# Kernel tuning notes

Measured on AMD Instinct MI355X. Metric: run time of the kernel, lower is better.

## Reference

```python
import math
import jax, jax.numpy as jnp
import numpy as np

B, L, INPUT_DIM, OUTPUT_DIM = 16, 4096, 7, 1
D_MODEL, N_HEADS, E_LAYERS, D_FF = 512, 8, 3, 2048
FACTOR, PRED_WIN = 5, 48


def layer_norm(x, g, b, eps=1e-5):
    m = x.mean(-1, keepdims=True)
    v = ((x - m) ** 2).mean(-1, keepdims=True)
    return (x - m) / jnp.sqrt(v + eps) * g + b


def prob_attention(q, k, v, key):
    # q,k,v: [B,H,L,d].  Canonical Informer ProbAttention, mask_flag=False.
    Bq, H, Lq, d = q.shape
    Lk = k.shape[2]
    sample_k = min(FACTOR * int(math.ceil(math.log(Lk))), Lk)
    n_top = min(FACTOR * int(math.ceil(math.log(Lq))), Lq)
    idx = jax.random.randint(key, (Lq, sample_k), 0, Lk)  # sampled key ids per query
    # sparsity measure M = max_s(QK_s) - mean(QK_s); indices carry no gradient
    qs = jax.lax.stop_gradient(q)
    ksg = jax.lax.stop_gradient(k)
    def body(carry, idx_s):
        m, s = carry
        ks = ksg[:, :, idx_s, :]                       # [B,H,Lq,d] gather
        qk = jnp.einsum('bhld,bhld->bhl', qs, ks)
        return (jnp.maximum(m, qk), s + qk), None
    init = (jnp.full((Bq, H, Lq), -jnp.inf, q.dtype), jnp.zeros((Bq, H, Lq), q.dtype))
    (m, s), _ = jax.lax.scan(body, init, idx.T)
    M = m - s / Lk
    top_idx = jax.lax.top_k(M, n_top)[1]               # [B,H,u] active queries
    q_red = jnp.take_along_axis(q, top_idx[..., None], axis=2)  # [B,H,u,d]
    scores = jnp.einsum('bhud,bhkd->bhuk', q_red, k) / jnp.sqrt(jnp.asarray(d, q.dtype))
    attn = jax.nn.softmax(scores, axis=-1)
    upd = jnp.einsum('bhuk,bhkd->bhud', attn, v)
    ctx = jnp.broadcast_to(v.mean(axis=2, keepdims=True), (Bq, H, Lq, d))
    bi = jnp.arange(Bq)[:, None, None]
    hi = jnp.arange(H)[None, :, None]
    return ctx.at[bi, hi, top_idx].set(upd)


def encoder_layer(x, Wq, bq, Wk, bk, Wv, bv, Wo, bo, W1, b1, W2, b2, g1, be1, g2, be2, key):
    Bx, Lx, D = x.shape
    H, d = N_HEADS, D // N_HEADS
    q = (x @ Wq + bq).reshape(Bx, Lx, H, d).transpose(0, 2, 1, 3)
    k = (x @ Wk + bk).reshape(Bx, Lx, H, d).transpose(0, 2, 1, 3)
    v = (x @ Wv + bv).reshape(Bx, Lx, H, d).transpose(0, 2, 1, 3)
    ctx = prob_attention(q, k, v, key)
    new_x = ctx.transpose(0, 2, 1, 3).reshape(Bx, Lx, D) @ Wo + bo
    x = layer_norm(x + new_x, g1, be1)
    y = jax.nn.gelu(x @ W1.T + b1, approximate=False)   # conv1d k=1 == linear
    y = y @ W2.T + b2
    return layer_norm(x + y, g2, be2)


def conv_layer(x, W, b, bn_g, bn_b):
    # Conv1d k=3 circular pad -> eval BatchNorm (mean 0, var 1) -> ELU -> MaxPool k=3 s=2 p=1
    xt = jnp.transpose(x, (0, 2, 1))                   # [B,C,L]
    xp = jnp.concatenate([xt[..., -1:], xt, xt[..., :1]], axis=-1)
    y = jax.lax.conv_general_dilated(xp, W, (1,), 'VALID', dimension_numbers=('NCH', 'OIH', 'NCH'))
    y = y + b[None, :, None]
    y = y / jnp.sqrt(1.0 + 1e-5) * bn_g[None, :, None] + bn_b[None, :, None]
    y = jax.nn.elu(y)
    yp = jnp.pad(y, ((0, 0), (0, 0), (1, 1)), constant_values=-jnp.inf)
    y = jax.lax.reduce_window(yp, -jnp.inf, jax.lax.max, (1, 1, 3), (1, 1, 2), 'VALID')
    return jnp.transpose(y, (0, 2, 1))                 # [B,L//2,C]


def setup_inputs() -> dict:
    key = jax.random.key(0)
    ks = jax.random.split(key, 12)
    s = 0.02
    f32 = jnp.float32
    return {
        'x': jax.random.normal(ks[0], (B, L, INPUT_DIM), f32),
        'emb_W': jax.random.normal(ks[1], (INPUT_DIM, D_MODEL), f32) * s,
        'emb_b': jnp.zeros((D_MODEL,), f32),
        'Wq': jax.random.normal(ks[2], (E_LAYERS, D_MODEL, D_MODEL), f32) * s,
        'bq': jnp.zeros((E_LAYERS, D_MODEL), f32),
        'Wk': jax.random.normal(ks[3], (E_LAYERS, D_MODEL, D_MODEL), f32) * s,
        'bk': jnp.zeros((E_LAYERS, D_MODEL), f32),
        'Wv': jax.random.normal(ks[4], (E_LAYERS, D_MODEL, D_MODEL), f32) * s,
        'bv': jnp.zeros((E_LAYERS, D_MODEL), f32),
        'Wo': jax.random.normal(ks[5], (E_LAYERS, D_MODEL, D_MODEL), f32) * s,
        'bo': jnp.zeros((E_LAYERS, D_MODEL), f32),
        'ff_W1': jax.random.normal(ks[6], (E_LAYERS, D_FF, D_MODEL), f32) * s,
        'ff_b1': jnp.zeros((E_LAYERS, D_FF), f32),
        'ff_W2': jax.random.normal(ks[7], (E_LAYERS, D_MODEL, D_FF), f32) * s,
        'ff_b2': jnp.zeros((E_LAYERS, D_MODEL), f32),
        'ln1_g': jnp.ones((E_LAYERS, D_MODEL), f32),
        'ln1_b': jnp.zeros((E_LAYERS, D_MODEL), f32),
        'ln2_g': jnp.ones((E_LAYERS, D_MODEL), f32),
        'ln2_b': jnp.zeros((E_LAYERS, D_MODEL), f32),
        'conv_W': jax.random.normal(ks[8], (E_LAYERS - 1, D_MODEL, D_MODEL, 3), f32) * s,
        'conv_b': jnp.zeros((E_LAYERS - 1, D_MODEL), f32),
        'bn_g': jnp.ones((E_LAYERS - 1, D_MODEL), f32),
        'bn_b': jnp.zeros((E_LAYERS - 1, D_MODEL), f32),
        'fln_g': jnp.ones((D_MODEL,), f32),
        'fln_b': jnp.zeros((D_MODEL,), f32),
        'proj_W': jax.random.normal(ks[9], (D_MODEL, OUTPUT_DIM), f32) * s,
        'proj_b': jnp.zeros((OUTPUT_DIM,), f32),
    }


def reference(x, emb_W, emb_b, Wq, bq, Wk, bk, Wv, bv, Wo, bo, ff_W1, ff_b1, ff_W2, ff_b2,
              ln1_g, ln1_b, ln2_g, ln2_b, conv_W, conv_b, bn_g, bn_b, fln_g, fln_b, proj_W, proj_b):
    h = x @ emb_W + emb_b
    base = jax.random.key(42)
    for i in range(E_LAYERS):
        h = encoder_layer(h, Wq[i], bq[i], Wk[i], bk[i], Wv[i], bv[i], Wo[i], bo[i],
                          ff_W1[i], ff_b1[i], ff_W2[i], ff_b2[i],
                          ln1_g[i], ln1_b[i], ln2_g[i], ln2_b[i],
                          jax.random.fold_in(base, i))
        if i < E_LAYERS - 1:
            h = conv_layer(h, conv_W[i], conv_b[i], bn_g[i], bn_b[i])
    h = layer_norm(h, fln_g, fln_b)
    out = h @ proj_W + proj_b
    return out[:, :PRED_WIN - 1, :]
```

## Files before the change

### kernel.cpp

```cpp
#include <hip/hip_runtime.h>
#include <cstdint>
#include <math.h>

#define NB 16
#define DM 512
#define NH 8
#define DFF_ 2048
#define SMAX 45

typedef unsigned short ushort_t;
typedef __bf16 bf16x8 __attribute__((ext_vector_type(8)));
typedef float f32x4 __attribute__((ext_vector_type(4)));

__device__ __forceinline__ ushort_t f2b(float f) {
  uint32_t u = __float_as_uint(f);
  uint32_t r = (u + 0x7FFFu + ((u >> 16) & 1u)) >> 16;
  return (ushort_t)r;
}
__device__ __forceinline__ float bu2f(ushort_t x) {
  return __uint_as_float((uint32_t)x << 16);
}
__device__ __forceinline__ float b2f_lo(uint32_t u) { return __uint_as_float(u << 16); }
__device__ __forceinline__ float b2f_hi(uint32_t u) { return __uint_as_float(u & 0xFFFF0000u); }
__device__ __forceinline__ uint32_t pack2(float lo, float hi) {
  return (uint32_t)f2b(lo) | ((uint32_t)f2b(hi) << 16);
}

__host__ __device__ inline void tf2x32(uint32_t k0, uint32_t k1,
                                       uint32_t x0, uint32_t x1,
                                       uint32_t* o0, uint32_t* o1) {
  uint32_t ks0 = k0, ks1 = k1, ks2 = k0 ^ k1 ^ 0x1BD11BDAu;
  x0 += ks0; x1 += ks1;
#define TF_RND(r) { x0 += x1; x1 = (x1 << (r)) | (x1 >> (32 - (r))); x1 ^= x0; }
  TF_RND(13) TF_RND(15) TF_RND(26) TF_RND(6)
  x0 += ks1; x1 += ks2 + 1u;
  TF_RND(17) TF_RND(29) TF_RND(16) TF_RND(24)
  x0 += ks2; x1 += ks0 + 2u;
  TF_RND(13) TF_RND(15) TF_RND(26) TF_RND(6)
  x0 += ks0; x1 += ks1 + 3u;
  TF_RND(17) TF_RND(29) TF_RND(16) TF_RND(24)
  x0 += ks1; x1 += ks2 + 4u;
  TF_RND(13) TF_RND(15) TF_RND(26) TF_RND(6)
  x0 += ks2; x1 += ks0 + 5u;
#undef TF_RND
  *o0 = x0; *o1 = x1;
}

__global__ void gen_idx_kernel(int* __restrict__ idx, uint32_t k0, uint32_t k1,
                               int n, int mask) {
  int j = blockIdx.x * 256 + threadIdx.x;
  if (j >= n) return;
  int half = n >> 1;
  uint32_t o0, o1;
  if (j < half) {
    tf2x32(k0, k1, (uint32_t)j, (uint32_t)(j + half), &o0, &o1);
    idx[j] = (int)(o0 & (uint32_t)mask);
  } else {
    tf2x32(k0, k1, (uint32_t)(j - half), (uint32_t)j, &o0, &o1);
    idx[j] = (int)(o1 & (uint32_t)mask);
  }
}

__device__ inline float blk_reduce_sum(float v) {
  __shared__ float s[4];
  for (int o = 32; o > 0; o >>= 1) v += __shfl_down(v, o);
  int lane = threadIdx.x & 63, w = threadIdx.x >> 6;
  if (lane == 0) s[w] = v;
  __syncthreads();
  float r = s[0] + s[1] + s[2] + s[3];
  __syncthreads();
  return r;
}

__global__ void embed_kernel(const float* __restrict__ x, const float* __restrict__ W,
                             const float* __restrict__ bias, ushort_t* __restrict__ h) {
  size_t gid = (size_t)blockIdx.x * 256 + threadIdx.x;
  int o4 = (int)(gid & 127) * 4;
  size_t bl = gid >> 7;
  const float* xr = x + bl * 7;
  float xv[7];
#pragma unroll
  for (int i = 0; i < 7; ++i) xv[i] = xr[i];
  float4 acc = *(const float4*)(bias + o4);
#pragma unroll
  for (int i = 0; i < 7; ++i) {
    float4 w4 = *(const float4*)(W + i * 512 + o4);
    acc.x += xv[i] * w4.x;
    acc.y += xv[i] * w4.y;
    acc.z += xv[i] * w4.z;
    acc.w += xv[i] * w4.w;
  }
  ushort4 o;
  o.x = f2b(acc.x); o.y = f2b(acc.y); o.z = f2b(acc.z); o.w = f2b(acc.w);
  *(ushort4*)(h + bl * 512 + o4) = o;
}

__global__ void cast_bf16(const float* __restrict__ src, ushort_t* __restrict__ dst,
                          size_t n) {
  size_t i = ((size_t)blockIdx.x * 256 + threadIdx.x) * 4;
  if (i >= n) return;
  float4 v = *(const float4*)(src + i);
  ushort4 o;
  o.x = f2b(v.x); o.y = f2b(v.y); o.z = f2b(v.z); o.w = f2b(v.w);
  *(ushort4*)(dst + i) = o;
}

__global__ void castT512(const float* __restrict__ W, ushort_t* __restrict__ Bt) {
  int gid = blockIdx.x * 256 + threadIdx.x;
  int n = gid >> 9, k = gid & 511;
  Bt[gid] = f2b(W[(size_t)k * 512 + n]);
}

__global__ void cast_convW(const float* __restrict__ W, ushort_t* __restrict__ Bt) {
  int gid = blockIdx.x * 256 + threadIdx.x;
  int n = gid / 1536, k = gid - n * 1536;
  int dt = k >> 9, ii = k & 511;
  Bt[gid] = f2b(W[((size_t)n * 512 + ii) * 3 + dt]);
}

__global__ void concat3(const float* __restrict__ a, const float* __restrict__ b,
                        const float* __restrict__ c, float* __restrict__ o) {
  int t = blockIdx.x * 256 + threadIdx.x;
  if (t >= 1536) return;
  o[t] = t < 512 ? a[t] : (t < 1024 ? b[t - 512] : c[t - 1024]);
}

__device__ __forceinline__ float gelu_exact(float c) {
  return 0.5f * c * (1.0f + erff(c * 0.70710678118654752f));
}

template <int MODE, int EPI>
__global__ __launch_bounds__(256) void mfma_gemm(
    const ushort_t* __restrict__ A, const ushort_t* __restrict__ Bt,
    const float* __restrict__ bias, float* __restrict__ Cf,
    ushort_t* __restrict__ Cb, const float* __restrict__ bng,
    const float* __restrict__ bnb, int N, int K, int L) {
  __shared__ __align__(16) ushort_t As[128 * 64];
  __shared__ __align__(16) ushort_t Bs[128 * 64];
  const int tid = threadIdx.x;
  const int lane = tid & 63;
  const int wid = tid >> 6;
  const int wr = wid >> 1, wc = wid & 1;
  const int bm = blockIdx.y, bn = blockIdx.x;
  const int ln = lane & 15, lh = lane >> 4;

  f32x4 acc[4][4] = {};

  for (int k0 = 0; k0 < K; k0 += 64) {
    __syncthreads();
#pragma unroll
    for (int it = 0; it < 4; ++it) {
      int c = it * 256 + tid;
      int row = c >> 3;
      int kc = (((c & 7) ^ (row & 7)) << 3);
      size_t ga;
      if (MODE == 1) {
        int m = bm * 128 + row;
        int b = m / L, tpos = m - b * L;
        int k = k0 + kc;
        int dt = k >> 9, ii = k & 511;
        int tr2 = tpos + dt - 1;
        if (tr2 < 0) tr2 += L;
        if (tr2 >= L) tr2 -= L;
        ga = ((size_t)(b * L + tr2)) * 512 + ii;
      } else {
        ga = (size_t)(bm * 128 + row) * K + k0 + kc;
      }
      __builtin_amdgcn_global_load_lds(
          (const __attribute__((address_space(1))) void*)(A + ga),
          (__attribute__((address_space(3))) void*)(As + c * 8), 16, 0, 0);
      size_t gb = (size_t)(bn * 128 + row) * K + k0 + kc;
      __builtin_amdgcn_global_load_lds(
          (const __attribute__((address_space(1))) void*)(Bt + gb),
          (__attribute__((address_space(3))) void*)(Bs + c * 8), 16, 0, 0);
    }
    __syncthreads();
#pragma unroll
    for (int kk = 0; kk < 2; ++kk) {
      bf16x8 af[4], bf_[4];
#pragma unroll
      for (int m = 0; m < 4; ++m) {
        int ar = wr * 64 + m * 16 + ln;
        int aoff = (kk * 32 + lh * 8) ^ ((ar & 7) << 3);
        af[m] = *(const bf16x8*)&As[ar * 64 + aoff];
      }
#pragma unroll
      for (int n = 0; n < 4; ++n) {
        int br = wc * 64 + n * 16 + ln;
        int boff = (kk * 32 + lh * 8) ^ ((br & 7) << 3);
        bf_[n] = *(const bf16x8*)&Bs[br * 64 + boff];
      }
#pragma unroll
      for (int m = 0; m < 4; ++m)
#pragma unroll
        for (int n = 0; n < 4; ++n)
          acc[m][n] =
              __builtin_amdgcn_mfma_f32_16x16x32_bf16(af[m], bf_[n], acc[m][n], 0, 0, 0);
    }
  }

  const float bnscale = 0.9999950000374996f;
#pragma unroll
  for (int m = 0; m < 4; ++m) {
    int row = bm * 128 + wr * 64 + m * 16 + lh * 4;
#pragma unroll
    for (int n = 0; n < 4; ++n) {
      int col = bn * 128 + wc * 64 + n * 16 + ln;
      float bsv = bias[col];
#pragma unroll
      for (int r = 0; r < 4; ++r) {
        float cval = acc[m][n][r] + bsv;
        if (MODE == 2) {
          ushort_t* dst = Cb + (size_t)(bn >> 2) * (size_t)L;
          dst[(size_t)(row + r) * 512 + (col & 511)] = f2b(cval);
        } else {
          size_t oi = (size_t)(row + r) * N + col;
          if (EPI == 0) {
            Cb[oi] = f2b(cval);
          } else if (EPI == 1) {
            Cb[oi] = f2b(cval + bu2f(Cb[oi]));
          } else if (EPI == 2) {
            Cb[oi] = f2b(gelu_exact(cval));
          } else {
            float c2 = cval * bnscale * bng[col] + bnb[col];
            Cf[oi] = c2 > 0.0f ? c2 : expm1f(c2);
          }
        }
      }
    }
  }
}

__global__ __launch_bounds__(256) void ln_inplace(ushort_t* __restrict__ h,
                                                  const float* __restrict__ g,
                                                  const float* __restrict__ b) {
  size_t row = blockIdx.x;
  uint32_t* hr = (uint32_t*)(h + row * 512);
  int t = threadIdx.x;
  uint32_t u = hr[t];
  float x0 = b2f_lo(u), x1 = b2f_hi(u);
  float mean = blk_reduce_sum(x0 + x1) * (1.0f / 512.0f);
  float d0 = x0 - mean, d1 = x1 - mean;
  float var = blk_reduce_sum(d0 * d0 + d1 * d1) * (1.0f / 512.0f);
  float rstd = rsqrtf(var + 1e-5f);
  float y0 = d0 * rstd * g[2 * t] + b[2 * t];
  float y1 = d1 * rstd * g[2 * t + 1] + b[2 * t + 1];
  hr[t] = pack2(y0, y1);
}

__global__ __launch_bounds__(256) void prob_scores_wave(const ushort_t* __restrict__ q,
                                                        const ushort_t* __restrict__ k,
                                                        const int* __restrict__ idx,
                                                        float* __restrict__ Mout,
                                                        int L, int S, int CBl) {
  int bid = blockIdx.x;
  int w = threadIdx.x >> 6;
  int lane = threadIdx.x & 63;
  int nxb = CBl < 8 ? CBl : 8;
  int gpb = 8 / nxb;
  int bmul = CBl / nxb;
  int xcd = bid & 7;
  int rest = bid >> 3;
  int b = (xcd / gpb) * bmul + (rest % bmul);
  int li = (rest / bmul) * gpb + (xcd % gpb);
  int l = li * 4 + w;

  const ushort_t* qr = q + ((size_t)(b * L + l)) * 512 + lane * 8;
  uint4 qu = *(const uint4*)qr;
  float qf[8];
  qf[0] = b2f_lo(qu.x); qf[1] = b2f_hi(qu.x);
  qf[2] = b2f_lo(qu.y); qf[3] = b2f_hi(qu.y);
  qf[4] = b2f_lo(qu.z); qf[5] = b2f_hi(qu.z);
  qf[6] = b2f_lo(qu.w); qf[7] = b2f_hi(qu.w);
  const int* il = idx + l * S;
  const ushort_t* kb = k + (size_t)b * L * 512 + lane * 8;
  float m = -INFINITY, ssum = 0.0f;
  for (int s = 0; s < S; ++s) {
    int j = il[s];
    uint4 ku = *(const uint4*)(kb + (size_t)j * 512);
    float dot = qf[0] * b2f_lo(ku.x) + qf[1] * b2f_hi(ku.x) +
                qf[2] * b2f_lo(ku.y) + qf[3] * b2f_hi(ku.y) +
                qf[4] * b2f_lo(ku.z) + qf[5] * b2f_hi(ku.z) +
                qf[6] * b2f_lo(ku.w) + qf[7] * b2f_hi(ku.w);
    dot += __shfl_xor(dot, 1);
    dot += __shfl_xor(dot, 2);
    dot += __shfl_xor(dot, 4);
    m = fmaxf(m, dot);
    ssum += dot;
  }
  if ((lane & 7) == 0) {
    int hh = lane >> 3;
    Mout[((size_t)(b * 8 + hh)) * L + l] = m - ssum / (float)L;
  }
}

__global__ __launch_bounds__(256) void topk_kernel(const float* __restrict__ Mbuf,
                                                   int* __restrict__ top_idx,
                                                   int L, int S) {
  int bh = blockIdx.x;
  __shared__ uint32_t keys[4096];
  __shared__ int hist[256];
  __shared__ int sh_bin, sh_found, sh_cnt;
  const float* Mr = Mbuf + (size_t)bh * L;
  int t = threadIdx.x;

  for (int j = t; j < L; j += 256) {
    uint32_t u = __float_as_uint(Mr[j]);
    keys[j] = (u & 0x80000000u) ? ~u : (u | 0x80000000u);
  }
  if (t == 0) sh_cnt = 0;
  __syncthreads();

  uint32_t prefix = 0;
  int found = 0;
  for (int p = 24; p >= 0; p -= 8) {
    hist[t] = 0;
    __syncthreads();
    for (int j = t; j < L; j += 256) {
      uint32_t key = keys[j];
      bool match = (p == 24) || ((key >> (p + 8)) == (prefix >> (p + 8)));
      if (match) atomicAdd(&hist[(key >> p) & 255], 1);
    }
    __syncthreads();
    for (int o = 1; o < 256; o <<= 1) {
      int add = (t + o < 256) ? hist[t + o] : 0;
      __syncthreads();
      hist[t] += add;
      __syncthreads();
    }
    int sufIncl = hist[t];
    int sufExcl = (t < 255) ? hist[t + 1] : 0;
    int needv = S - found;
    if (sufExcl < needv && needv <= sufIncl) { sh_bin = t; sh_found = found + sufExcl; }
    __syncthreads();
    prefix |= (uint32_t)sh_bin << p;
    found = sh_found;
    __syncthreads();
  }

  uint32_t tau = prefix;
  int r = S - found;
  int chunk = L >> 8;
  int base = t * chunk;
  int localEq = 0;
  for (int i = 0; i < chunk; ++i) localEq += (keys[base + i] == tau) ? 1 : 0;
  hist[t] = localEq;
  __syncthreads();
  for (int o = 1; o < 256; o <<= 1) {
    int add = (t >= o) ? hist[t - o] : 0;
    __syncthreads();
    hist[t] += add;
    __syncthreads();
  }
  int myRank = hist[t] - localEq;
  for (int i = 0; i < chunk; ++i) {
    uint32_t key = keys[base + i];
    bool isEq = (key == tau);
    bool sel = (key > tau) || (isEq && myRank < r);
    if (isEq) myRank++;
    if (sel) {
      int slot = atomicAdd(&sh_cnt, 1);
      top_idx[bh * S + slot] = base + i;
    }
  }
}

__global__ __launch_bounds__(256) void mean_v_partial(const ushort_t* __restrict__ v,
                                                      float* __restrict__ part, int L) {
  int b = blockIdx.x;
  int chunk = blockIdx.y;
  int t = threadIdx.x;
  int c = t * 2;
  const ushort_t* base = v + ((size_t)b * L + (size_t)chunk * 256) * 512 + c;
  float a0 = 0.0f, a1 = 0.0f;
#pragma unroll 8
  for (int r = 0; r < 256; ++r) {
    uint32_t u = *(const uint32_t*)(base + (size_t)r * 512);
    a0 += b2f_lo(u);
    a1 += b2f_hi(u);
  }
  float* p = part + ((size_t)b * 16 + chunk) * 512 + c;
  p[0] = a0;
  p[1] = a1;
}

__global__ void mean_v_finish(const float* __restrict__ part, float* __restrict__ mv,
                              int L, int nchunks) {
  int b = blockIdx.x;
  int c = threadIdx.x;
  float s = 0.0f;
  for (int k = 0; k < nchunks; ++k) s += part[((size_t)b * 16 + k) * 512 + c];
  mv[b * 512 + c] = s / (float)L;
}

__global__ void fill_ctx(ushort_t* __restrict__ ctx, const float* __restrict__ mv,
                         int L) {
  size_t gid = (size_t)blockIdx.x * 256 + threadIdx.x;
  int c = (int)(gid & 511);
  size_t bl = gid >> 9;
  int b = (int)(bl / (size_t)L);
  ctx[gid] = f2b(mv[b * 512 + c]);
}

__global__ __launch_bounds__(256) void flash_attn(const ushort_t* __restrict__ q,
                                                  const ushort_t* __restrict__ k,
                                                  const ushort_t* __restrict__ v,
                                                  const int* __restrict__ top_idx,
                                                  float* __restrict__ pz,
                                                  float* __restrict__ po,
                                                  int L, int S, int CBNH) {
  __shared__ float qs[SMAX * 64];
  __shared__ ushort_t pt[SMAX * 64];
  int bh = blockIdx.y, js = blockIdx.x;
  int hh = bh & 7, b = bh >> 3;
  int t = threadIdx.x;
  int lane = t & 63, w = t >> 6;
  for (int e = t; e < S * 64; e += 256) {
    int u = e >> 6, d = e & 63;
    int l = top_idx[bh * S + u];
    qs[e] = bu2f(q[((size_t)(b * L + l)) * 512 + hh * 64 + d]);
  }
  __syncthreads();
  int j0 = js * 64;
  const ushort_t* kr = k + ((size_t)(b * L + j0 + lane)) * 512 + hh * 64;
  uint4 kreg[8];
#pragma unroll
  for (int c = 0; c < 8; ++c) kreg[c] = ((const uint4*)kr)[c];
  float zs[12];
#pragma unroll
  for (int mi = 0; mi < 12; ++mi) {
    int u = w + mi * 4;
    if (u < S) {
      const float* qu = qs + u * 64;
      float dot = 0.0f;
#pragma unroll
      for (int c = 0; c < 8; ++c) {
        uint4 ku = kreg[c];
        const float* q8 = qu + c * 8;
        dot += q8[0] * b2f_lo(ku.x) + q8[1] * b2f_hi(ku.x) +
               q8[2] * b2f_lo(ku.y) + q8[3] * b2f_hi(ku.y) +
               q8[4] * b2f_lo(ku.z) + q8[5] * b2f_hi(ku.z) +
               q8[6] * b2f_lo(ku.w) + q8[7] * b2f_hi(ku.w);
      }
      float P = __expf(dot * 0.125f);
      ushort_t Pb = f2b(P);
      pt[u * 64 + lane] = Pb;
      float ps = bu2f(Pb);
#pragma unroll
      for (int o2 = 1; o2 < 64; o2 <<= 1) ps += __shfl_xor(ps, o2);
      zs[mi] = ps;
    }
  }
  __syncthreads();
  float oacc[12] = {};
  for (int jb = 0; jb < 64; jb += 4) {
    float vv[4];
#pragma unroll
    for (int r = 0; r < 4; ++r)
      vv[r] = bu2f(v[((size_t)(b * L + j0 + jb + r)) * 512 + hh * 64 + lane]);
#pragma unroll
    for (int mi = 0; mi < 12; ++mi) {
      int u = w + mi * 4;
      if (u < S) {
        const ushort_t* p4 = &pt[u * 64 + jb];
        oacc[mi] += bu2f(p4[0]) * vv[0] + bu2f(p4[1]) * vv[1] +
                    bu2f(p4[2]) * vv[2] + bu2f(p4[3]) * vv[3];
      }
    }
  }
  size_t base = (size_t)js * CBNH + bh;
#pragma unroll
  for (int mi = 0; mi < 12; ++mi) {
    int u = w + mi * 4;
    if (u < S) {
      po[(base * SMAX + u) * 64 + lane] = oacc[mi];
      if (lane == 0) pz[base * SMAX + u] = zs[mi];
    }
  }
}

__global__ void flash_finish(const float* __restrict__ pz, const float* __restrict__ po,
                             const int* __restrict__ top_idx, ushort_t* __restrict__ ctx,
                             int L, int S, int CBNH, int fj) {
  int gid = blockIdx.x * 256 + threadIdx.x;
  if (gid >= CBNH * S * 64) return;
  int d = gid & 63;
  int r = gid >> 6;
  int u = r % S, bh = r / S;
  int hh = bh & 7, b = bh >> 3;
  float Z = 0.0f, O = 0.0f;
  for (int js = 0; js < fj; ++js) {
    size_t pi = ((size_t)js * CBNH + bh) * SMAX + u;
    Z += pz[pi];
    O += po[pi * 64 + d];
  }
  int l = top_idx[bh * S + u];
  ctx[((size_t)(b * L + l)) * 512 + hh * 64 + d] = f2b(O / Z);
}

__global__ void maxpool_kernel(const float* __restrict__ y, ushort_t* __restrict__ hout,
                               int L) {
  size_t gid = (size_t)blockIdx.x * 256 + threadIdx.x;
  int Lh = L >> 1;
  int o = (int)(gid & 511);
  size_t bj = gid >> 9;
  int j = (int)(bj % (size_t)Lh);
  int b = (int)(bj / (size_t)Lh);
  const float* base = y + ((size_t)(b * L + 2 * j)) * 512 + o;
  float mx = base[0];
  if (j > 0) mx = fmaxf(mx, base[-512]);
  mx = fmaxf(mx, base[512]);
  hout[gid] = f2b(mx);
}

__global__ __launch_bounds__(256) void final_ln_proj(const ushort_t* __restrict__ h,
                                                     const float* __restrict__ g,
                                                     const float* __restrict__ bb,
                                                     const float* __restrict__ pw,
                                                     const float* __restrict__ pb,
                                                     float* __restrict__ out, int L) {
  int b = blockIdx.x / 47, l = blockIdx.x % 47;
  const uint32_t* hr = (const uint32_t*)(h + ((size_t)(b * L + l)) * 512);
  int t = threadIdx.x;
  uint32_t u = hr[t];
  float x0 = b2f_lo(u), x1 = b2f_hi(u);
  float mean = blk_reduce_sum(x0 + x1) * (1.0f / 512.0f);
  float d0 = x0 - mean, d1 = x1 - mean;
  float var = blk_reduce_sum(d0 * d0 + d1 * d1) * (1.0f / 512.0f);
  float rstd = rsqrtf(var + 1e-5f);
  float y0 = d0 * rstd * g[2 * t] + bb[2 * t];
  float y1 = d1 * rstd * g[2 * t + 1] + bb[2 * t + 1];
  float dot = blk_reduce_sum(y0 * pw[2 * t] + y1 * pw[2 * t + 1]);
  if (t == 0) out[b * 47 + l] = dot + pb[0];
}

extern "C" void kernel_launch(void* const* d_in, const int* in_sizes, int n_in,
                              void* d_out, int out_size, void* d_ws, size_t ws_size,
                              hipStream_t stream) {
  const float* x = (const float*)d_in[0];
  const float* emb_W = (const float*)d_in[1];
  const float* emb_b = (const float*)d_in[2];
  const float* Wq = (const float*)d_in[3];
  const float* bq = (const float*)d_in[4];
  const float* Wk = (const float*)d_in[5];
  const float* bk = (const float*)d_in[6];
  const float* Wv = (const float*)d_in[7];
  const float* bv = (const float*)d_in[8];
  const float* Wo = (const float*)d_in[9];
  const float* bo = (const float*)d_in[10];
  const float* fW1 = (const float*)d_in[11];
  const float* fb1 = (const float*)d_in[12];
  const float* fW2 = (const float*)d_in[13];
  const float* fb2 = (const float*)d_in[14];
  const float* ln1g = (const float*)d_in[15];
  const float* ln1b = (const float*)d_in[16];
  const float* ln2g = (const float*)d_in[17];
  const float* ln2b = (const float*)d_in[18];
  const float* cW = (const float*)d_in[19];
  const float* cb = (const float*)d_in[20];
  const float* bng = (const float*)d_in[21];
  const float* bnb = (const float*)d_in[22];
  const float* flng = (const float*)d_in[23];
  const float* flnb = (const float*)d_in[24];
  const float* pW = (const float*)d_in[25];
  const float* pb = (const float*)d_in[26];
  float* out = (float*)d_out;

  int CB0 = 16;
  while (CB0 > 1) {
    size_t need = 19086848ull + (size_t)CB0 * 5724672ull;
    if (need * 4 <= ws_size) break;
    CB0 >>= 1;
  }
  const size_t CBseg = (size_t)CB0 * 2097152ull;

  float* ws = (float*)d_ws;
  size_t off = 0;
  ushort_t* h = (ushort_t*)ws;             off += 16777216ull;
  ushort_t* wbase = (ushort_t*)(ws + off); off += 1966080ull;
  ushort_t* WqkvT = wbase;
  ushort_t* WoT = wbase + 786432;
  ushort_t* W1b = wbase + 1048576;
  ushort_t* W2b = wbase + 2097152;
  ushort_t* Wcb = wbase + 3145728;
  float* bqkv = ws + off;                  off += 1536ull;
  ushort_t* gArea = (ushort_t*)(ws + off); off += 2ull * CBseg;
  ushort_t* qb = gArea;
  ushort_t* kbuf = gArea + CBseg;
  ushort_t* vb = gArea + 2 * CBseg;
  ushort_t* ctxb = gArea + 3 * CBseg;
  ushort_t* ybuf = gArea;
  float* convY = (float*)gArea;
  float* Mbuf = ws + off;                  off += (size_t)CB0 * 32768;
  float* mv = ws + off;                    off += 8192ull;
  int* topidx = (int*)(ws + off);          off += 6144ull;
  int* idxbuf = (int*)(ws + off);          off += 196608ull;
  float* pzb = ws + off;                   off += (size_t)CB0 * 23040;
  float* pob = ws + off;                   off += (size_t)CB0 * 1474560;
  float* mvpart = ws + off;                off += 131072ull;

  {
    size_t total = (size_t)NB * 4096 * 128;
    embed_kernel<<<(int)(total / 256), 256, 0, stream>>>(x, emb_W, emb_b, h);
  }

  int L = 4096;
  for (int i = 0; i < 3; ++i) {
    int S = (i == 0) ? 45 : (i == 1) ? 40 : 35;
    int CBl = CB0 * (4096 / L);
    if (CBl > NB) CBl = NB;
    int ngroups = NB / CBl;
    int CBNHl = CBl * NH;
    int Mg = CBl * L;
    size_t segL = (size_t)Mg * 512;
    int fj = L / 64;

    castT512<<<1024, 256, 0, stream>>>(Wq + (size_t)i * 262144, WqkvT);
    castT512<<<1024, 256, 0, stream>>>(Wk + (size_t)i * 262144, WqkvT + 262144);
    castT512<<<1024, 256, 0, stream>>>(Wv + (size_t)i * 262144, WqkvT + 524288);
    castT512<<<1024, 256, 0, stream>>>(Wo + (size_t)i * 262144, WoT);
    cast_bf16<<<1024, 256, 0, stream>>>(fW1 + (size_t)i * 1048576, W1b, 1048576);
    cast_bf16<<<1024, 256, 0, stream>>>(fW2 + (size_t)i * 1048576, W2b, 1048576);
    if (i < 2) cast_convW<<<3072, 256, 0, stream>>>(cW + (size_t)i * 786432, Wcb);
    concat3<<<6, 256, 0, stream>>>(bq + i * DM, bk + i * DM, bv + i * DM, bqkv);

    uint32_t fa, fbk;
    tf2x32(0u, 42u, 0u, (uint32_t)i, &fa, &fbk);
    uint32_t a0, b0, a1, b1;
    tf2x32(fa, fbk, 0u, 2u, &a0, &b0);
    tf2x32(fa, fbk, 1u, 3u, &a1, &b1);
    int n = L * S;
    gen_idx_kernel<<<(n + 255) / 256, 256, 0, stream>>>(idxbuf, b0, b1, n, L - 1);

    for (int g = 0; g < ngroups; ++g) {
      ushort_t* hg = h + (size_t)g * segL;
      dim3 gqkv(12, Mg / 128);
      mfma_gemm<2, 0><<<gqkv, 256, 0, stream>>>(hg, WqkvT, bqkv, nullptr, qb,
                                                nullptr, nullptr, 1536, 512,
                                                (int)CBseg);

      prob_scores_wave<<<(CBl * L) / 4, 256, 0, stream>>>(qb, kbuf, idxbuf, Mbuf,
                                                          L, S, CBl);
      topk_kernel<<<CBNHl, 256, 0, stream>>>(Mbuf, topidx, L, S);

      mean_v_partial<<<dim3(CBl, L / 256), 256, 0, stream>>>(vb, mvpart, L);
      mean_v_finish<<<CBl, 512, 0, stream>>>(mvpart, mv, L, L / 256);
      fill_ctx<<<(int)(segL / 256), 256, 0, stream>>>(ctxb, mv, L);
      flash_attn<<<dim3(fj, CBNHl), 256, 0, stream>>>(qb, kbuf, vb, topidx,
                                                      pzb, pob, L, S, CBNHl);
      flash_finish<<<(CBNHl * S * 64 + 255) / 256, 256, 0, stream>>>(
          pzb, pob, topidx, ctxb, L, S, CBNHl, fj);

      dim3 gq(4, Mg / 128);
      mfma_gemm<0, 1><<<gq, 256, 0, stream>>>(ctxb, WoT, bo + i * DM, nullptr, hg,
                                              nullptr, nullptr, 512, 512, 0);
    }
    ln_inplace<<<NB * L, 256, 0, stream>>>(h, ln1g + i * DM, ln1b + i * DM);

    int rows = NB * L;
    int R = CB0 * 4096;
    if (R > rows) R = rows;
    for (int r0 = 0; r0 < rows; r0 += R) {
      ushort_t* hr = h + (size_t)r0 * 512;
      dim3 g1(16, R / 128);
      mfma_gemm<0, 2><<<g1, 256, 0, stream>>>(hr, W1b, fb1 + i * DFF_, nullptr, ybuf,
                                              nullptr, nullptr, 2048, 512, 0);
      dim3 g2(4, R / 128);
      mfma_gemm<0, 1><<<g2, 256, 0, stream>>>(ybuf, W2b, fb2 + i * DM, nullptr, hr,
                                              nullptr, nullptr, 512, 2048, 0);
    }
    ln_inplace<<<NB * L, 256, 0, stream>>>(h, ln2g + i * DM, ln2b + i * DM);

    if (i < 2) {
      int Lh = L / 2;
      for (int g = 0; g < ngroups; ++g) {
        ushort_t* hg = h + (size_t)g * segL;
        dim3 gc(4, Mg / 128);
        mfma_gemm<1, 3><<<gc, 256, 0, stream>>>(hg, Wcb, cb + i * DM, convY, nullptr,
                                                bng + i * DM, bnb + i * DM, 512, 1536, L);
        size_t tot = (size_t)CBl * Lh * 512;
        maxpool_kernel<<<(int)(tot / 256), 256, 0, stream>>>(
            convY, h + (size_t)g * CBl * Lh * 512, L);
      }
      L = Lh;
    }
  }

  final_ln_proj<<<NB * 47, 256, 0, stream>>>(h, flng, flnb, pW, pb, out, L);
}
```

Baseline: 3.085 ms.

## Rewrite top-query attention partials with bf16 MFMA and swizzled LDS tiles

Result: faster. 2.713 ms (-12.1%).

```diff
diff --git a/kernel.cpp b/kernel.cpp
--- a/kernel.cpp
+++ b/kernel.cpp
@@ -409,74 +409,95 @@
                                                   float* __restrict__ pz,
                                                   float* __restrict__ po,
                                                   int L, int S, int CBNH) {
-  __shared__ float qs[SMAX * 64];
-  __shared__ ushort_t pt[SMAX * 64];
+  __shared__ __align__(16) ushort_t qs[48 * 64];
+  __shared__ __align__(16) ushort_t Kt[64 * 64];
+  __shared__ __align__(16) ushort_t Vt[64 * 64];
+  __shared__ __align__(16) ushort_t Ps[48 * 64];
+  __shared__ float zpart[4][48];
   int bh = blockIdx.y, js = blockIdx.x;
   int hh = bh & 7, b = bh >> 3;
   int t = threadIdx.x;
   int lane = t & 63, w = t >> 6;
-  for (int e = t; e < S * 64; e += 256) {
-    int u = e >> 6, d = e & 63;
-    int l = top_idx[bh * S + u];
-    qs[e] = bu2f(q[((size_t)(b * L + l)) * 512 + hh * 64 + d]);
+  int ln = lane & 15, lh = lane >> 4;
+  int j0 = js * 64;
+
+  for (int e = t; e < 48 * 8; e += 256) {
+    int u = e >> 3, c = e & 7;
+    uint4 val = make_uint4(0u, 0u, 0u, 0u);
+    if (u < S) {
+      int l = top_idx[bh * S + u];
+      val = *(const uint4*)(q + ((size_t)(b * L + l)) * 512 + hh * 64 + c * 8);
+    }
+    *(uint4*)(qs + u * 64 + ((c ^ (u & 7)) << 3)) = val;
+  }
+  for (int e = t; e < 64 * 8; e += 256) {
+    int j = e >> 3, c = e & 7;
+    uint4 kv = *(const uint4*)(k + ((size_t)(b * L + j0 + j)) * 512 + hh * 64 + c * 8);
+    *(uint4*)(Kt + j * 64 + ((c ^ (j & 7)) << 3)) = kv;
+    uint4 vv = *(const uint4*)(v + ((size_t)(b * L + j0 + j)) * 512 + hh * 64 + c * 8);
+    const ushort_t* pv8 = (const ushort_t*)&vv;
+#pragma unroll
+    for (int ee = 0; ee < 8; ++ee) {
+      int d = c * 8 + ee;
+      Vt[d * 64 + (((j >> 3) ^ (d & 7)) << 3) + (j & 7)] = pv8[ee];
+    }
   }
   __syncthreads();
-  int j0 = js * 64;
-  const ushort_t* kr = k + ((size_t)(b * L + j0 + lane)) * 512 + hh * 64;
-  uint4 kreg[8];
-#pragma unroll
-  for (int c = 0; c < 8; ++c) kreg[c] = ((const uint4*)kr)[c];
-  float zs[12];
-#pragma unroll
-  for (int mi = 0; mi < 12; ++mi) {
-    int u = w + mi * 4;
-    if (u < S) {
-      const float* qu = qs + u * 64;
-      float dot = 0.0f;
-#pragma unroll
-      for (int c = 0; c < 8; ++c) {
-        uint4 ku = kreg[c];
-        const float* q8 = qu + c * 8;
-        dot += q8[0] * b2f_lo(ku.x) + q8[1] * b2f_hi(ku.x) +
-               q8[2] * b2f_lo(ku.y) + q8[3] * b2f_hi(ku.y) +
-               q8[4] * b2f_lo(ku.z) + q8[5] * b2f_hi(ku.z) +
-               q8[6] * b2f_lo(ku.w) + q8[7] * b2f_hi(ku.w);
-      }
-      float P = __expf(dot * 0.125f);
+
+  f32x4 sacc[3] = {};
+#pragma unroll
+  for (int kk = 0; kk < 2; ++kk) {
+    int j = w * 16 + ln;
+    bf16x8 bfr = *(const bf16x8*)&Kt[j * 64 + (((kk * 4 + lh) ^ (j & 7)) << 3)];
+#pragma unroll
+    for (int qm = 0; qm < 3; ++qm) {
+      int u = qm * 16 + ln;
+      bf16x8 af = *(const bf16x8*)&qs[u * 64 + (((kk * 4 + lh) ^ (u & 7)) << 3)];
+      sacc[qm] = __builtin_amdgcn_mfma_f32_16x16x32_bf16(af, bfr, sacc[qm], 0, 0, 0);
+    }
+  }
+#pragma unroll
+  for (int qm = 0; qm < 3; ++qm) {
+#pragma unroll
+    for (int r = 0; r < 4; ++r) {
+      int u = qm * 16 + lh * 4 + r;
+      float P = __expf(sacc[qm][r] * 0.125f);
       ushort_t Pb = f2b(P);
-      pt[u * 64 + lane] = Pb;
+      int key = w * 16 + ln;
+      Ps[u * 64 + (((key >> 3) ^ (u & 7)) << 3) + (key & 7)] = Pb;
       float ps = bu2f(Pb);
-#pragma unroll
-      for (int o2 = 1; o2 < 64; o2 <<= 1) ps += __shfl_xor(ps, o2);
-      zs[mi] = ps;
+      ps += __shfl_xor(ps, 1);
+      ps += __shfl_xor(ps, 2);
+      ps += __shfl_xor(ps, 4);
+      ps += __shfl_xor(ps, 8);
+      if (ln == 0) zpart[w][u] = ps;
     }
   }
   __syncthreads();
-  float oacc[12] = {};
-  for (int jb = 0; jb < 64; jb += 4) {
-    float vv[4];
-#pragma unroll
-    for (int r = 0; r < 4; ++r)
-      vv[r] = bu2f(v[((size_t)(b * L + j0 + jb + r)) * 512 + hh * 64 + lane]);
-#pragma unroll
-    for (int mi = 0; mi < 12; ++mi) {
-      int u = w + mi * 4;
-      if (u < S) {
-        const ushort_t* p4 = &pt[u * 64 + jb];
-        oacc[mi] += bu2f(p4[0]) * vv[0] + bu2f(p4[1]) * vv[1] +
-                    bu2f(p4[2]) * vv[2] + bu2f(p4[3]) * vv[3];
-      }
+
+  f32x4 oacc[3] = {};
+#pragma unroll
+  for (int kk = 0; kk < 2; ++kk) {
+    int d = w * 16 + ln;
+    bf16x8 bfr = *(const bf16x8*)&Vt[d * 64 + (((kk * 4 + lh) ^ (d & 7)) << 3)];
+#pragma unroll
+    for (int qm = 0; qm < 3; ++qm) {
+      int u = qm * 16 + ln;
+      bf16x8 af = *(const bf16x8*)&Ps[u * 64 + (((kk * 4 + lh) ^ (u & 7)) << 3)];
+      oacc[qm] = __builtin_amdgcn_mfma_f32_16x16x32_bf16(af, bfr, oacc[qm], 0, 0, 0);
     }
   }
   size_t base = (size_t)js * CBNH + bh;
 #pragma unroll
-  for (int mi = 0; mi < 12; ++mi) {
-    int u = w + mi * 4;
-    if (u < S) {
-      po[(base * SMAX + u) * 64 + lane] = oacc[mi];
-      if (lane == 0) pz[base * SMAX + u] = zs[mi];
-    }
-  }
+  for (int qm = 0; qm < 3; ++qm) {
+#pragma unroll
+    for (int r = 0; r < 4; ++r) {
+      int u = qm * 16 + lh * 4 + r;
+      if (u < S) po[(base * SMAX + u) * 64 + w * 16 + ln] = oacc[qm][r];
+    }
+  }
+  if (t < S) pz[base * SMAX + t] =
+      zpart[0][t] + zpart[1][t] + zpart[2][t] + zpart[3][t];
 }
 
 __global__ void flash_finish(const float* __restrict__ pz, const float* __restrict__ po,
```
